# Optimization experiments

Measured on AMD Instinct MI355X. Metric: run time of the kernel, lower is better.

The kernel has to match this reference:

```python
import jax, jax.numpy as jnp
import numpy as np

BS, TLEN, NNODE, DIM = 32, 6, 4, 1500
HID = 128; D2 = 2 * HID
LSTMH, LSTMO, KCONV = 64, 128, 3
CONV_OUT = 191
DECAY = 0.7
WIN, STRIDES = (2, 2), (1, 2)
FEAT_IN = LSTMO * CONV_OUT  # 24448


def _bn(x, p, axis):
    # eval-mode BatchNorm: p = [gamma, beta, running_mean, running_var] stacked [4, C]
    sh = [1] * x.ndim; sh[axis] = -1
    g, b, m, v = (p[i].reshape(sh) for i in range(4))
    return (x - m) * (g * jax.lax.rsqrt(v + 1e-5)) + b


def _conv1d(x, w, pad):  # x [B,C,L], w [O,I,K]
    return jax.lax.conv_general_dilated(x, w, (1,), [(pad, pad)],
                                        dimension_numbers=('NCH', 'OIH', 'NCH'))


def _maxpool2(x):  # MaxPool1d(kernel=2, stride=2, padding=1) with -inf padding
    x = jnp.pad(x, ((0, 0), (0, 0), (1, 1)), constant_values=-jnp.inf)
    return jax.lax.reduce_window(x, -jnp.inf, jax.lax.max, (1, 1, 2), (1, 1, 2), 'VALID')


def _mpnn_block(x, w, s, gw, gb, bnA, tw, tb, bnM):
    # x: [bs, tlen, ns, d]; Conv_GraphST windowing + dot-graph + masked adj + 1-hop MPNN + mean pool
    bs, tlen, ns, d = x.shape
    nw = (tlen - w) // s + 1
    con = jnp.stack([x[:, j * s:j * s + w] for j in range(nw)], axis=1)  # [bs,nw,w,ns,d]
    Xc = con.reshape(bs * nw, w * ns, d)  # node index = t*ns + sensor (time-major)
    f = Xc @ gw + gb
    N = w * ns
    eye = jnp.eye(N, dtype=x.dtype)
    Adj = jnp.einsum('bnd,bmd->bnm', f, f)
    Adj = jax.nn.softmax(jax.nn.leaky_relu(Adj - eye * 1e8), axis=-1) + eye
    t = jnp.arange(N) // ns
    mask = DECAY ** jnp.abs(t[:, None] - t[None, :]).astype(x.dtype)  # Mask_Matrix decay
    Adj = Adj * mask
    Xb = _bn(Xc, bnA, -1)  # BN over feature channel (transpose-BN-transpose in torch)
    h = jnp.einsum('bnm,bmd->bnd', Adj, Xb) @ tw + tb
    h = jax.nn.leaky_relu(_bn(h, bnM, -1))
    return h.reshape(bs, nw, w, ns, -1).mean(axis=2)  # mean pool over window-time


def _pos_encoding(tlen, d):
    pos = jnp.arange(tlen, dtype=jnp.float32)[:, None]
    div = jnp.exp(jnp.arange(0, d, 2, dtype=jnp.float32) * (-np.log(100.0) / d))
    pe = jnp.zeros((tlen, d), jnp.float32)
    return pe.at[:, 0::2].set(jnp.sin(pos * div)).at[:, 1::2].set(jnp.cos(pos * div))


def reference(X, conv1_w, bn1, conv2_w, bn2, conv3_w, bn3,
              map2_w, map2_b, bn_map2,
              g1_w, g1_b, bnA1, th1_w, th1_b, bnM1,
              g2_w, g2_b, bnA2, th2_w, th2_b, bnM2,
              fc1_w, fc1_b, fc2_w, fc2_b, fc3_w, fc3_b, fc4_w, fc4_b):
    X = X.reshape(BS, TLEN, NNODE, -1)
    B = BS * TLEN * NNODE
    a = jnp.transpose(X.reshape(B, -1, 1), (0, 2, 1))  # [B,1,L]
    a = _maxpool2(jax.nn.relu(_bn(_conv1d(a, conv1_w, KCONV // 2), bn1, 1)))
    a = _maxpool2(jax.nn.relu(_bn(_conv1d(a, conv2_w, 2), bn2, 1)))
    a = _maxpool2(jax.nn.relu(_bn(_conv1d(a, conv3_w, 3), bn3, 1)))  # [B,LSTMO,CONV_OUT]
    a = a.reshape(B, -1)
    a = _bn(a @ map2_w + map2_b, bn_map2, -1)
    a = a.reshape(BS, TLEN, NNODE, D2)
    a = a + _pos_encoding(TLEN, D2)[None, :, None, :]  # PE over time, per (batch, node)
    out1 = _mpnn_block(a, WIN[0], STRIDES[0], g1_w, g1_b, bnA1, th1_w, th1_b, bnM1)  # [32,5,4,128]
    out2 = _mpnn_block(a, WIN[1], STRIDES[1], g2_w, g2_b, bnA2, th2_w, th2_b, bnM2)  # [32,3,4,128]
    feats = jnp.concatenate([out1.reshape(BS, -1), out2.reshape(BS, -1)], axis=-1)  # [32,4096]
    h = jax.nn.relu(feats @ fc1_w + fc1_b)
    h = jax.nn.relu(h @ fc2_w + fc2_b)
    h = jax.nn.relu(h @ fc3_w + fc3_b)
    return h @ fc4_w + fc4_b


def setup_inputs():
    key = jax.random.key(0)
    ks = iter(jax.random.split(key, 80))
    def rn(shape, scale=1.0):
        return scale * jax.random.normal(next(ks), shape, jnp.float32)
    def bn(c):
        return jnp.stack([1.0 + 0.1 * rn((c,)), 0.1 * rn((c,)), 0.1 * rn((c,)),
                          1.0 + 0.5 * jax.random.uniform(next(ks), (c,), jnp.float32)])
    def lin(i, o):
        return rn((i, o), 1.0 / np.sqrt(i))
    return {
        'X': rn((BS, TLEN, NNODE, DIM)),
        'conv1_w': rn((LSTMH, 1, KCONV), 0.3),
        'bn1': bn(LSTMH),
        'conv2_w': rn((2 * LSTMH, LSTMH, KCONV), 1.0 / np.sqrt(LSTMH * KCONV)),
        'bn2': bn(2 * LSTMH),
        'conv3_w': rn((LSTMO, 2 * LSTMH, KCONV), 1.0 / np.sqrt(2 * LSTMH * KCONV)),
        'bn3': bn(LSTMO),
        'map2_w': lin(FEAT_IN, D2), 'map2_b': rn((D2,), 0.01), 'bn_map2': bn(D2),
        'g1_w': lin(D2, D2), 'g1_b': rn((D2,), 0.01), 'bnA1': bn(D2),
        'th1_w': lin(D2, HID), 'th1_b': rn((HID,), 0.01), 'bnM1': bn(HID),
        'g2_w': lin(D2, D2), 'g2_b': rn((D2,), 0.01), 'bnA2': bn(D2),
        'th2_w': lin(D2, HID), 'th2_b': rn((HID,), 0.01), 'bnM2': bn(HID),
        'fc1_w': lin(4096, D2), 'fc1_b': rn((D2,), 0.01),
        'fc2_w': lin(D2, D2), 'fc2_b': rn((D2,), 0.01),
        'fc3_w': lin(D2, HID), 'fc3_b': rn((HID,), 0.01),
        'fc4_w': lin(HID, 5), 'fc4_b': rn((5,), 0.01),
    }
```

## Files before the change

### kernel.cpp

```cpp
#include <hip/hip_runtime.h>
#include <hip/hip_bf16.h>

#define L1X   1500
#define L1P   751
#define C1    64
#define L2P   377
#define C2    128
#define L3P   191
#define C3    128
#define FEATK 24448
#define D2    256
#define HIDN  128
#define KSTEPS 764
#define CHUNK 192

typedef __attribute__((ext_vector_type(8))) short bf16x8;
typedef __attribute__((ext_vector_type(4))) float f32x4;

__device__ __forceinline__ short f2bf(float x) {
    union { float f; unsigned u; } v; v.f = x;
    unsigned r = (v.u + 0x7FFFu + ((v.u >> 16) & 1u)) >> 16;
    return (short)r;
}
__device__ __forceinline__ float bf2f(short s) {
    union { float f; unsigned u; } v; v.u = ((unsigned)(unsigned short)s) << 16;
    return v.f;
}

template<int IC, int KB>
__global__ __launch_bounds__(256)
void k_wprep(const float* __restrict__ w, short* __restrict__ WtHi,
             short* __restrict__ WtLo)
{
    int idx = blockIdx.x * 256 + threadIdx.x;
    if (idx >= 3 * KB * 4 * 128 * 8) return;
    int i    = idx & 7;
    int rest = idx >> 3;
    int c    = rest & 127; rest >>= 7;
    int sub  = rest & 3;   rest >>= 2;
    int kb   = rest % KB;
    int tap  = rest / KB;
    int ic   = kb * 32 + sub * 8 + i;
    float x  = w[(c * IC + ic) * 3 + tap];
    short h  = f2bf(x);
    WtHi[idx] = h;
    WtLo[idx] = f2bf(x - bf2f(h));
}

__global__ __launch_bounds__(256)
void k_wmprep(const float* __restrict__ W, short* __restrict__ Wmhi,
              short* __restrict__ Wmlo)
{
    const int ks  = blockIdx.x >> 2;
    const int sub = blockIdx.x & 3;
    const int n   = threadIdx.x;
    const int kbase = ks * 32 + sub * 8;
    bf16x8 vh, vl;
    #pragma unroll
    for (int i = 0; i < 8; ++i) {
        int k = kbase + i;
        int c = k & 127, ip = k >> 7;
        float x = W[(size_t)(c * 191 + ip) * D2 + n];
        short h = f2bf(x);
        vh[i] = h;
        vl[i] = f2bf(x - bf2f(h));
    }
    size_t off = ((size_t)(ks * 4 + sub) * 256 + n) * 8;
    *(bf16x8*)(Wmhi + off) = vh;
    *(bf16x8*)(Wmlo + off) = vl;
}

__global__ __launch_bounds__(256)
void k_zero(float* __restrict__ p, int n)
{
    int i = blockIdx.x * 256 + threadIdx.x;
    if (i < n) p[i] = 0.f;
}

template<int IC, int KB, int CONVLEN, int POOLLEN, bool HL>
__device__ __forceinline__
void conv_mfma_core(const short* __restrict__ WtHi, const short* __restrict__ WtLo,
                    const short* lhi, const short* llo,
                    const float* sc, const float* bc,
                    float* __restrict__ outp, short* __restrict__ ohi,
                    short* __restrict__ olo, int P0)
{
    const int lane = threadIdx.x & 63;
    const int wave = threadIdx.x >> 6;
    const int l15  = lane & 15;
    const int sub  = lane >> 4;

    f32x4 acc[2][8];
    #pragma unroll
    for (int mf = 0; mf < 2; ++mf)
        #pragma unroll
        for (int nf = 0; nf < 8; ++nf)
            acc[mf][nf] = (f32x4){0.f, 0.f, 0.f, 0.f};

    #pragma unroll
    for (int tap = 0; tap < 3; ++tap) {
        #pragma unroll
        for (int kb = 0; kb < KB; ++kb) {
            bf16x8 ah[2], al[2];
            #pragma unroll
            for (int mf = 0; mf < 2; ++mf) {
                int r = wave * 32 + mf * 16 + l15 + tap;
                int chunk = (kb * 4 + sub) ^ (r & 7);
                int off = r * IC + chunk * 8;
                ah[mf] = *(const bf16x8*)(lhi + off);
                al[mf] = *(const bf16x8*)(llo + off);
            }
            const short* wbh = WtHi + (size_t)(((tap * KB + kb) * 4 + sub) * 128) * 8;
            const short* wbl = WtLo + (size_t)(((tap * KB + kb) * 4 + sub) * 128) * 8;
            #pragma unroll
            for (int nf = 0; nf < 8; ++nf) {
                bf16x8 bh = *(const bf16x8*)(wbh + (nf * 16 + l15) * 8);
                bf16x8 bl = *(const bf16x8*)(wbl + (nf * 16 + l15) * 8);
                #pragma unroll
                for (int mf = 0; mf < 2; ++mf) {
                    acc[mf][nf] = __builtin_amdgcn_mfma_f32_16x16x32_bf16(ah[mf], bh, acc[mf][nf], 0, 0, 0);
                    acc[mf][nf] = __builtin_amdgcn_mfma_f32_16x16x32_bf16(ah[mf], bl, acc[mf][nf], 0, 0, 0);
                    acc[mf][nf] = __builtin_amdgcn_mfma_f32_16x16x32_bf16(al[mf], bh, acc[mf][nf], 0, 0, 0);
                }
            }
        }
    }

    #pragma unroll
    for (int mf = 0; mf < 2; ++mf) {
        int mbase = wave * 32 + mf * 16 + sub * 4;
        #pragma unroll
        for (int nf = 0; nf < 8; ++nf) {
            int c = nf * 16 + l15;
            float s = sc[c], bb = bc[c];
            float v[4];
            #pragma unroll
            for (int rg = 0; rg < 4; ++rg) {
                int p = P0 + mbase + rg;
                float x = fmaxf(acc[mf][nf][rg] * s + bb, 0.f);
                v[rg] = (p >= 0 && p < CONVLEN) ? x : 0.f;
            }
            int i0 = (P0 + mbase + 1) >> 1;
            float u0 = fmaxf(v[0], v[1]);
            float u1 = fmaxf(v[2], v[3]);
            if constexpr (HL) {
                if (i0 < POOLLEN) {
                    short h = f2bf(u0);
                    ohi[(size_t)i0 * 128 + c] = h;
                    olo[(size_t)i0 * 128 + c] = f2bf(u0 - bf2f(h));
                }
                if (i0 + 1 < POOLLEN) {
                    short h = f2bf(u1);
                    ohi[(size_t)(i0 + 1) * 128 + c] = h;
                    olo[(size_t)(i0 + 1) * 128 + c] = f2bf(u1 - bf2f(h));
                }
            } else {
                if (i0 < POOLLEN)     outp[(size_t)i0 * 128 + c] = u0;
                if (i0 + 1 < POOLLEN) outp[(size_t)(i0 + 1) * 128 + c] = u1;
            }
        }
    }
}

__global__ __launch_bounds__(256)
void k_conv2_mfma(const float* __restrict__ X, const float* __restrict__ w1,
                  const float* __restrict__ bn1,
                  const short* __restrict__ Wt2hi, const short* __restrict__ Wt2lo,
                  const float* __restrict__ bn2, short* __restrict__ p2hi,
                  short* __restrict__ p2lo, int b_off)
{
    const int blk = blockIdx.x;
    const int bl  = blk / 6, t = blk % 6;
    const int b   = b_off + bl;
    const int P0  = 128 * t - 1;
    const int T0  = 128 * t - 3;
    const int X0  = 256 * t - 8;

    __shared__ __align__(16) float xw[264];
    __shared__ __align__(16) short t1h[130 * 64];
    __shared__ __align__(16) short t1l[130 * 64];
    __shared__ float sb1s[64], sb1b[64], sc2[128], bc2[128];

    const int tid = threadIdx.x;
    for (int g = tid; g < 262; g += 256) {
        int xi = X0 + g;
        xw[g] = (xi >= 0 && xi < L1X) ? X[(size_t)b * L1X + xi] : 0.f;
    }
    if (tid < 64) {
        float s = bn1[tid] * rsqrtf(bn1[192 + tid] + 1e-5f);
        sb1s[tid] = s;
        sb1b[tid] = bn1[64 + tid] - bn1[128 + tid] * s;
    }
    if (tid < 128) {
        float s = bn2[tid] * rsqrtf(bn2[384 + tid] + 1e-5f);
        sc2[tid] = s;
        bc2[tid] = bn2[128 + tid] - bn2[256 + tid] * s;
    }
    __syncthreads();

    for (int idx = tid; idx < 130 * 64; idx += 256) {
        int r = idx >> 6, c = idx & 63;
        int tt = T0 + r;
        float val = 0.f;
        if (tt >= 0 && tt <= 750) {
            float wk0 = w1[c * 3], wk1 = w1[c * 3 + 1], wk2 = w1[c * 3 + 2];
            float s = sb1s[c], bias = sb1b[c];
            float v0 = 0.f, v1 = 0.f;
            int li = 2 * r;
            if (tt >= 1)
                v0 = fmaxf((wk0 * xw[li] + wk1 * xw[li + 1] + wk2 * xw[li + 2]) * s + bias, 0.f);
            if (tt <= 749)
                v1 = fmaxf((wk0 * xw[li + 1] + wk1 * xw[li + 2] + wk2 * xw[li + 3]) * s + bias, 0.f);
            val = fmaxf(v0, v1);
        }
        short h = f2bf(val);
        int chunk = (c >> 3) ^ (r & 7);
        int off = r * 64 + chunk * 8 + (c & 7);
        t1h[off] = h;
        t1l[off] = f2bf(val - bf2f(h));
    }
    __syncthreads();

    conv_mfma_core<64, 2, 753, 377, true>(Wt2hi, Wt2lo, t1h, t1l, sc2, bc2,
                                          nullptr,
                                          p2hi + (size_t)bl * L2P * 128,
                                          p2lo + (size_t)bl * L2P * 128, P0);
}

__global__ __launch_bounds__(256)
void k_conv3_mfma(const short* __restrict__ p2hi, const short* __restrict__ p2lo,
                  const short* __restrict__ Wt3hi, const short* __restrict__ Wt3lo,
                  const float* __restrict__ bn3, short* __restrict__ p3hi,
                  short* __restrict__ p3lo, int b_off)
{
    const int blk = blockIdx.x;
    const int bl  = blk / 3, t = blk % 3;
    const int b   = b_off + bl;
    const int P0  = 128 * t - 1;
    const int I0  = 128 * t - 4;

    __shared__ __align__(16) short t2h[130 * 128];
    __shared__ __align__(16) short t2l[130 * 128];
    __shared__ float sc3[128], bc3[128];

    const int tid = threadIdx.x;
    if (tid < 128) {
        float s = bn3[tid] * rsqrtf(bn3[384 + tid] + 1e-5f);
        sc3[tid] = s;
        bc3[tid] = bn3[128 + tid] - bn3[256 + tid] * s;
    }

    const short* s2h = p2hi + (size_t)bl * L2P * 128;
    const short* s2l = p2lo + (size_t)bl * L2P * 128;
    for (int idx = tid; idx < 130 * 32; idx += 256) {
        int r = idx >> 5, q = idx & 31;
        int pr = I0 + r;
        short4 vh = make_short4(0, 0, 0, 0), vl = make_short4(0, 0, 0, 0);
        if (pr >= 0 && pr < L2P) {
            vh = *(const short4*)(s2h + (size_t)pr * 128 + q * 4);
            vl = *(const short4*)(s2l + (size_t)pr * 128 + q * 4);
        }
        int chunk = (q >> 1) ^ (r & 7);
        int off = r * 128 + chunk * 8 + (q & 1) * 4;
        *(short4*)(t2h + off) = vh;
        *(short4*)(t2l + off) = vl;
    }
    __syncthreads();

    conv_mfma_core<128, 4, 381, 191, true>(Wt3hi, Wt3lo, t2h, t2l, sc3, bc3,
                                           nullptr,
                                           p3hi + (size_t)b * FEATK,
                                           p3lo + (size_t)b * FEATK, P0);
}

__global__ __launch_bounds__(256)
void k_map2_mfma(const short* __restrict__ Ahi, const short* __restrict__ Alo,
                 const short* __restrict__ Wmhi, const short* __restrict__ Wmlo,
                 float* __restrict__ accum)
{
    const int kt   = blockIdx.x % 48;
    const int mt   = blockIdx.x / 48;
    const int tid  = threadIdx.x;
    const int lane = tid & 63, wave = tid >> 6;
    const int l15  = lane & 15, sub = lane >> 4;
    const int wm   = wave >> 1, wn = wave & 1;
    const int m0   = mt * 64;

    const int s0 = kt * 16;
    const int s1 = (s0 + 16 < KSTEPS) ? s0 + 16 : KSTEPS;

    __shared__ __align__(16) short Ah[2][64 * 40];
    __shared__ __align__(16) short Al[2][64 * 40];

    const int r  = tid >> 2;
    const int kb = tid & 3;
    const size_t abase = (size_t)(m0 + r) * FEATK + kb * 8;
    const int    lbase = r * 40 + kb * 8;

    f32x4 acc[2][8];
    #pragma unroll
    for (int mf = 0; mf < 2; ++mf)
        #pragma unroll
        for (int nf = 0; nf < 8; ++nf)
            acc[mf][nf] = (f32x4){0.f, 0.f, 0.f, 0.f};

    *(bf16x8*)&Ah[0][lbase] = *(const bf16x8*)(Ahi + abase + (size_t)s0 * 32);
    *(bf16x8*)&Al[0][lbase] = *(const bf16x8*)(Alo + abase + (size_t)s0 * 32);

    int cur = 0;
    for (int s = s0; s < s1; ++s) {
        __syncthreads();
        if (s + 1 < s1) {
            *(bf16x8*)&Ah[cur ^ 1][lbase] = *(const bf16x8*)(Ahi + abase + (size_t)(s + 1) * 32);
            *(bf16x8*)&Al[cur ^ 1][lbase] = *(const bf16x8*)(Alo + abase + (size_t)(s + 1) * 32);
        }
        bf16x8 ah[2], al[2];
        #pragma unroll
        for (int mf = 0; mf < 2; ++mf) {
            int off = (wm * 32 + mf * 16 + l15) * 40 + sub * 8;
            ah[mf] = *(const bf16x8*)&Ah[cur][off];
            al[mf] = *(const bf16x8*)&Al[cur][off];
        }
        const short* wb = Wmhi + ((size_t)(s * 4 + sub) * 256 + wn * 128) * 8;
        const short* wl = Wmlo + ((size_t)(s * 4 + sub) * 256 + wn * 128) * 8;
        #pragma unroll
        for (int nf = 0; nf < 8; ++nf) {
            bf16x8 bh = *(const bf16x8*)(wb + (nf * 16 + l15) * 8);
            bf16x8 bl = *(const bf16x8*)(wl + (nf * 16 + l15) * 8);
            #pragma unroll
            for (int mf = 0; mf < 2; ++mf) {
                acc[mf][nf] = __builtin_amdgcn_mfma_f32_16x16x32_bf16(ah[mf], bh, acc[mf][nf], 0, 0, 0);
                acc[mf][nf] = __builtin_amdgcn_mfma_f32_16x16x32_bf16(ah[mf], bl, acc[mf][nf], 0, 0, 0);
                acc[mf][nf] = __builtin_amdgcn_mfma_f32_16x16x32_bf16(al[mf], bh, acc[mf][nf], 0, 0, 0);
            }
        }
        cur ^= 1;
    }

    float* acct = accum + (size_t)(kt & 7) * 196608;
    #pragma unroll
    for (int mf = 0; mf < 2; ++mf) {
        int mrow = m0 + wm * 32 + mf * 16 + sub * 4;
        #pragma unroll
        for (int nf = 0; nf < 8; ++nf) {
            int n = wn * 128 + nf * 16 + l15;
            #pragma unroll
            for (int rg = 0; rg < 4; ++rg)
                atomicAdd(&acct[(size_t)(mrow + rg) * D2 + n], acc[mf][nf][rg]);
        }
    }
}

__global__ __launch_bounds__(256)
void k_map2fin(const float* __restrict__ accum, const float* __restrict__ mb,
               const float* __restrict__ bn, float* __restrict__ out)
{
    const int row = blockIdx.x;
    const int n   = threadIdx.x;
    float acc = 0.f;
    #pragma unroll
    for (int c = 0; c < 8; ++c)
        acc += accum[(size_t)c * 196608 + (size_t)row * D2 + n];

    float s    = bn[n] * rsqrtf(bn[768 + n] + 1e-5f);
    float beta = bn[256 + n];
    float mu   = bn[512 + n];
    float bias = mb[n];
    int   jj   = n >> 1;
    float freq = expf((float)(2 * jj) * (-4.605170185988092f / 256.f));
    int   t    = (row >> 2) % 6;
    float ang  = (float)t * freq;
    float pe   = (n & 1) ? cosf(ang) : sinf(ang);
    out[(size_t)row * D2 + n] = (acc + bias - mu) * s + beta + pe;
}

__global__ __launch_bounds__(256)
void k_mpnn(const float* __restrict__ a_pe, const float* __restrict__ gw,
            const float* __restrict__ gb, const float* __restrict__ bnA,
            const float* __restrict__ tw, const float* __restrict__ tb_,
            const float* __restrict__ bnM, float* __restrict__ feats,
            int nw, int stride, int base)
{
    const int g  = blockIdx.x;
    const int b  = g / nw, wi = g % nw;
    const int tid = threadIdx.x;

    __shared__ float Xc[8][256];
    __shared__ float Xb[8][256];
    __shared__ float Fs[8][256];
    __shared__ float Adj[8][8];
    __shared__ float hsm[8][128];

    for (int e = tid; e < 2048; e += 256) {
        int nn = e >> 8, d = e & 255;
        int tt = nn >> 2, sn = nn & 3;
        float v = a_pe[(((size_t)(b * 6) + (wi * stride + tt)) * 4 + sn) * D2 + d];
        Xc[nn][d] = v;
        float s = bnA[d] * rsqrtf(bnA[768 + d] + 1e-5f);
        Xb[nn][d] = (v - bnA[512 + d]) * s + bnA[256 + d];
    }
    __syncthreads();

    {
        const int d = tid;
        #pragma unroll
        for (int nn = 0; nn < 8; ++nn) {
            float acc = gb[d];
            for (int k = 0; k < 256; ++k) acc += Xc[nn][k] * gw[(size_t)k * D2 + d];
            Fs[nn][d] = acc;
        }
    }
    __syncthreads();

    if (tid < 64) {
        int nn = tid >> 3, m = tid & 7;
        float s = 0.f;
        for (int d = 0; d < 256; ++d) s += Fs[nn][d] * Fs[m][d];
        if (nn == m) s -= 1e8f;
        s = (s > 0.f) ? s : 0.01f * s;
        Adj[nn][m] = s;
    }
    __syncthreads();

    if (tid < 8) {
        int nn = tid;
        float mx = -1e30f;
        for (int m = 0; m < 8; ++m) mx = fmaxf(mx, Adj[nn][m]);
        float ex[8]; float sum = 0.f;
        for (int m = 0; m < 8; ++m) { ex[m] = expf(Adj[nn][m] - mx); sum += ex[m]; }
        float inv = 1.f / sum;
        for (int m = 0; m < 8; ++m) {
            float v = ex[m] * inv + ((nn == m) ? 1.f : 0.f);
            v *= ((nn >> 2) == (m >> 2)) ? 1.f : 0.7f;
            Adj[nn][m] = v;
        }
    }
    __syncthreads();

    {
        const int d = tid;
        float hm[8];
        #pragma unroll
        for (int nn = 0; nn < 8; ++nn) {
            float a = 0.f;
            #pragma unroll
            for (int m = 0; m < 8; ++m) a += Adj[nn][m] * Xb[m][d];
            hm[nn] = a;
        }
        #pragma unroll
        for (int nn = 0; nn < 8; ++nn) Fs[nn][d] = hm[nn];
    }
    __syncthreads();

    {
        const int o = tid & 127, half = tid >> 7;
        float ms  = bnM[o] * rsqrtf(bnM[384 + o] + 1e-5f);
        float mbe = bnM[128 + o], mmu = bnM[256 + o];
        #pragma unroll
        for (int q = 0; q < 4; ++q) {
            int nn = half + 2 * q;
            float acc = tb_[o];
            for (int d = 0; d < 256; ++d) acc += Fs[nn][d] * tw[(size_t)d * HIDN + o];
            float y = (acc - mmu) * ms + mbe;
            hsm[nn][o] = (y > 0.f) ? y : 0.01f * y;
        }
    }
    __syncthreads();

    for (int e = tid; e < 512; e += 256) {
        int sn = e >> 7, o = e & 127;
        feats[(size_t)b * 4096 + base + (wi * 4 + sn) * HIDN + o] =
            0.5f * (hsm[sn][o] + hsm[4 + sn][o]);
    }
}

__global__ __launch_bounds__(256)
void k_fc1(const float* __restrict__ feats, const float* __restrict__ w1f,
           float* __restrict__ partfc)
{
    const int kc = blockIdx.x >> 3;
    const int nc = blockIdx.x & 7;
    const int tid = threadIdx.x;

    __shared__ float fst[32 * 257];

    for (int idx = tid; idx < 32 * 256; idx += 256) {
        int r = idx >> 8, k = idx & 255;
        fst[r * 257 + k] = feats[(size_t)r * 4096 + kc * 256 + k];
    }
    __syncthreads();

    const int c  = tid & 31;
    const int rg = tid >> 5;
    const float* wp = w1f + (size_t)(kc * 256) * 256 + nc * 32 + c;

    float acc[4] = {0.f, 0.f, 0.f, 0.f};
    for (int k = 0; k < 256; ++k) {
        float wv = wp[(size_t)k * 256];
        #pragma unroll
        for (int j = 0; j < 4; ++j)
            acc[j] += fst[(rg * 4 + j) * 257 + k] * wv;
    }
    #pragma unroll
    for (int j = 0; j < 4; ++j)
        partfc[((size_t)kc * 32 + rg * 4 + j) * 256 + nc * 32 + c] = acc[j];
}

__global__ __launch_bounds__(256)
void k_fc_rest(const float* __restrict__ partfc,
               const float* __restrict__ b1f,
               const float* __restrict__ w2f, const float* __restrict__ b2f,
               const float* __restrict__ w3f, const float* __restrict__ b3f,
               const float* __restrict__ w4f, const float* __restrict__ b4f,
               float* __restrict__ out)
{
    const int b = blockIdx.x;
    const int n = threadIdx.x;
    __shared__ float h1[256], h2[256], h3[128];

    {
        float acc = b1f[n];
        #pragma unroll
        for (int kc = 0; kc < 16; ++kc)
            acc += partfc[((size_t)kc * 32 + b) * 256 + n];
        h1[n] = fmaxf(acc, 0.f);
    }
    __syncthreads();
    {
        float acc = b2f[n];
        for (int k = 0; k < 256; ++k) acc += h1[k] * w2f[(size_t)k * 256 + n];
        h2[n] = fmaxf(acc, 0.f);
    }
    __syncthreads();
    if (n < 128) {
        float acc = b3f[n];
        for (int k = 0; k < 256; ++k) acc += h2[k] * w3f[(size_t)k * 128 + n];
        h3[n] = fmaxf(acc, 0.f);
    }
    __syncthreads();
    if (n < 5) {
        float acc = b4f[n];
        for (int k = 0; k < 128; ++k) acc += h3[k] * w4f[(size_t)k * 5 + n];
        out[b * 5 + n] = acc;
    }
}

extern "C" void kernel_launch(void* const* d_in, const int* in_sizes, int n_in,
                              void* d_out, int out_size, void* d_ws, size_t ws_size,
                              hipStream_t stream)
{
    const float* X      = (const float*)d_in[0];
    const float* w1     = (const float*)d_in[1];
    const float* bn1    = (const float*)d_in[2];
    const float* w2     = (const float*)d_in[3];
    const float* bn2    = (const float*)d_in[4];
    const float* w3     = (const float*)d_in[5];
    const float* bn3    = (const float*)d_in[6];
    const float* map2w  = (const float*)d_in[7];
    const float* map2b  = (const float*)d_in[8];
    const float* bnm2   = (const float*)d_in[9];
    const float* g1w    = (const float*)d_in[10];
    const float* g1b    = (const float*)d_in[11];
    const float* bnA1   = (const float*)d_in[12];
    const float* th1w   = (const float*)d_in[13];
    const float* th1b   = (const float*)d_in[14];
    const float* bnM1   = (const float*)d_in[15];
    const float* g2w    = (const float*)d_in[16];
    const float* g2b    = (const float*)d_in[17];
    const float* bnA2   = (const float*)d_in[18];
    const float* th2w   = (const float*)d_in[19];
    const float* th2b   = (const float*)d_in[20];
    const float* bnM2   = (const float*)d_in[21];
    const float* fc1w   = (const float*)d_in[22];
    const float* fc1b   = (const float*)d_in[23];
    const float* fc2w   = (const float*)d_in[24];
    const float* fc2b   = (const float*)d_in[25];
    const float* fc3w   = (const float*)d_in[26];
    const float* fc3b   = (const float*)d_in[27];
    const float* fc4w   = (const float*)d_in[28];
    const float* fc4b   = (const float*)d_in[29];
    float* out = (float*)d_out;

    float* ws = (float*)d_ws;
    const size_t SZ_P2 = (size_t)CHUNK * L2P * 128;
    short* p2hi  = (short*)ws;
    short* p2lo  = p2hi + SZ_P2;
    short* Wmhi  = (short*)ws;
    short* Wmlo  = Wmhi + 6258688;
    float* accum = (float*)(Wmlo + 6258688);
    float* after  = ws + 9264384;
    short* p3hi   = (short*)after;
    short* p3lo   = p3hi + 18776064;
    float* a_pe   = (float*)(p3lo + 18776064);
    float* feats  = a_pe + 196608;
    short* Wt2hi  = (short*)(feats + 131072);
    short* Wt2lo  = Wt2hi + 24576;
    short* Wt3hi  = Wt2lo + 24576;
    short* Wt3lo  = Wt3hi + 49152;
    float* partfc = (float*)(Wt3lo + 49152);

    k_wprep<64, 2><<<96, 256, 0, stream>>>(w2, Wt2hi, Wt2lo);
    k_wprep<128, 4><<<192, 256, 0, stream>>>(w3, Wt3hi, Wt3lo);

    for (int boff = 0; boff < 768; boff += CHUNK) {
        k_conv2_mfma<<<CHUNK * 6, 256, 0, stream>>>(X, w1, bn1, Wt2hi, Wt2lo, bn2,
                                                    p2hi, p2lo, boff);
        k_conv3_mfma<<<CHUNK * 3, 256, 0, stream>>>(p2hi, p2lo, Wt3hi, Wt3lo, bn3,
                                                    p3hi, p3lo, boff);
    }
    k_wmprep<<<KSTEPS * 4, 256, 0, stream>>>(map2w, Wmhi, Wmlo);
    k_zero<<<(8 * 196608 + 255) / 256, 256, 0, stream>>>(accum, 8 * 196608);
    k_map2_mfma<<<576, 256, 0, stream>>>(p3hi, p3lo, Wmhi, Wmlo, accum);
    k_map2fin<<<768, 256, 0, stream>>>(accum, map2b, bnm2, a_pe);
    k_mpnn<<<160, 256, 0, stream>>>(a_pe, g1w, g1b, bnA1, th1w, th1b, bnM1,
                                    feats, 5, 1, 0);
    k_mpnn<<<96, 256, 0, stream>>>(a_pe, g2w, g2b, bnA2, th2w, th2b, bnM2,
                                   feats, 3, 2, 2560);
    k_fc1<<<128, 256, 0, stream>>>(feats, fc1w, partfc);
    k_fc_rest<<<32, 256, 0, stream>>>(partfc, fc1b, fc2w, fc2b, fc3w, fc3b,
                                      fc4w, fc4b, out);
}
```

Measured before the change: 679.0 us.

## Stage conv epilogue through LDS, vectorize conv1 and conv3 loads, merge MPNN launches

The conv MFMA epilogue now writes pooled bf16 hi/lo results into the shared input tile and then copies them to global memory as 16-byte vectors, replacing scattered 2-byte stores. The conv1 stage computes four channels per thread with float4 weight loads and short4 stores. The conv3 tile load is batched into registers with clamped addresses before being written to LDS. The two MPNN launches are merged into one grid. Together these aim to cut uncoalesced store traffic and launch overhead, at the cost of extra barriers and higher register pressure from the 17-entry staging arrays.

```diff
diff --git a/kernel.cpp b/kernel.cpp
--- a/kernel.cpp
+++ b/kernel.cpp
@@ -77,13 +77,12 @@
     if (i < n) p[i] = 0.f;
 }
 
-template<int IC, int KB, int CONVLEN, int POOLLEN, bool HL>
+template<int IC, int KB, int CONVLEN, int POOLLEN>
 __device__ __forceinline__
 void conv_mfma_core(const short* __restrict__ WtHi, const short* __restrict__ WtLo,
-                    const short* lhi, const short* llo,
+                    short* lhi, short* llo,
                     const float* sc, const float* bc,
-                    float* __restrict__ outp, short* __restrict__ ohi,
-                    short* __restrict__ olo, int P0)
+                    short* __restrict__ ohi, short* __restrict__ olo, int P0)
 {
     const int lane = threadIdx.x & 63;
     const int wave = threadIdx.x >> 6;
@@ -126,9 +125,11 @@
         }
     }
 
+    __syncthreads();
     #pragma unroll
     for (int mf = 0; mf < 2; ++mf) {
         int mbase = wave * 32 + mf * 16 + sub * 4;
+        int lr = mbase >> 1;
         #pragma unroll
         for (int nf = 0; nf < 8; ++nf) {
             int c = nf * 16 + l15;
@@ -140,24 +141,25 @@
                 float x = fmaxf(acc[mf][nf][rg] * s + bb, 0.f);
                 v[rg] = (p >= 0 && p < CONVLEN) ? x : 0.f;
             }
-            int i0 = (P0 + mbase + 1) >> 1;
             float u0 = fmaxf(v[0], v[1]);
             float u1 = fmaxf(v[2], v[3]);
-            if constexpr (HL) {
-                if (i0 < POOLLEN) {
-                    short h = f2bf(u0);
-                    ohi[(size_t)i0 * 128 + c] = h;
-                    olo[(size_t)i0 * 128 + c] = f2bf(u0 - bf2f(h));
-                }
-                if (i0 + 1 < POOLLEN) {
-                    short h = f2bf(u1);
-                    ohi[(size_t)(i0 + 1) * 128 + c] = h;
-                    olo[(size_t)(i0 + 1) * 128 + c] = f2bf(u1 - bf2f(h));
-                }
-            } else {
-                if (i0 < POOLLEN)     outp[(size_t)i0 * 128 + c] = u0;
-                if (i0 + 1 < POOLLEN) outp[(size_t)(i0 + 1) * 128 + c] = u1;
-            }
+            short h0 = f2bf(u0), h1 = f2bf(u1);
+            lhi[lr * 128 + c]       = h0;
+            llo[lr * 128 + c]       = f2bf(u0 - bf2f(h0));
+            lhi[(lr + 1) * 128 + c] = h1;
+            llo[(lr + 1) * 128 + c] = f2bf(u1 - bf2f(h1));
+        }
+    }
+    __syncthreads();
+
+    const int i0base = (P0 + 1) >> 1;
+    for (int e = threadIdx.x; e < 1024; e += 256) {
+        int row = e >> 4, g = e & 15;
+        if (i0base + row < POOLLEN) {
+            *(bf16x8*)(ohi + (size_t)(i0base + row) * 128 + g * 8) =
+                *(const bf16x8*)(lhi + row * 128 + g * 8);
+            *(bf16x8*)(olo + (size_t)(i0base + row) * 128 + g * 8) =
+                *(const bf16x8*)(llo + row * 128 + g * 8);
         }
     }
 }
@@ -198,33 +200,44 @@
     }
     __syncthreads();
 
-    for (int idx = tid; idx < 130 * 64; idx += 256) {
-        int r = idx >> 6, c = idx & 63;
+    for (int q2 = tid; q2 < 130 * 16; q2 += 256) {
+        int r  = q2 >> 4;
+        int cq = (q2 & 15) * 4;
         int tt = T0 + r;
-        float val = 0.f;
+        short4 sh = make_short4(0, 0, 0, 0), sl = make_short4(0, 0, 0, 0);
         if (tt >= 0 && tt <= 750) {
-            float wk0 = w1[c * 3], wk1 = w1[c * 3 + 1], wk2 = w1[c * 3 + 2];
-            float s = sb1s[c], bias = sb1b[c];
-            float v0 = 0.f, v1 = 0.f;
             int li = 2 * r;
-            if (tt >= 1)
-                v0 = fmaxf((wk0 * xw[li] + wk1 * xw[li + 1] + wk2 * xw[li + 2]) * s + bias, 0.f);
-            if (tt <= 749)
-                v1 = fmaxf((wk0 * xw[li + 1] + wk1 * xw[li + 2] + wk2 * xw[li + 3]) * s + bias, 0.f);
-            val = fmaxf(v0, v1);
-        }
-        short h = f2bf(val);
-        int chunk = (c >> 3) ^ (r & 7);
-        int off = r * 64 + chunk * 8 + (c & 7);
-        t1h[off] = h;
-        t1l[off] = f2bf(val - bf2f(h));
-    }
-    __syncthreads();
-
-    conv_mfma_core<64, 2, 753, 377, true>(Wt2hi, Wt2lo, t1h, t1l, sc2, bc2,
-                                          nullptr,
-                                          p2hi + (size_t)bl * L2P * 128,
-                                          p2lo + (size_t)bl * L2P * 128, P0);
+            float xa = xw[li], xb = xw[li + 1], xc = xw[li + 2], xd = xw[li + 3];
+            float4 wA = *(const float4*)(w1 + cq * 3);
+            float4 wB = *(const float4*)(w1 + cq * 3 + 4);
+            float4 wC = *(const float4*)(w1 + cq * 3 + 8);
+            float wv[4][3] = {{wA.x, wA.y, wA.z}, {wA.w, wB.x, wB.y},
+                              {wB.z, wB.w, wC.x}, {wC.y, wC.z, wC.w}};
+            #pragma unroll
+            for (int j = 0; j < 4; ++j) {
+                int c = cq + j;
+                float s = sb1s[c], bias = sb1b[c];
+                float v0 = 0.f, v1 = 0.f;
+                if (tt >= 1)
+                    v0 = fmaxf((wv[j][0] * xa + wv[j][1] * xb + wv[j][2] * xc) * s + bias, 0.f);
+                if (tt <= 749)
+                    v1 = fmaxf((wv[j][0] * xb + wv[j][1] * xc + wv[j][2] * xd) * s + bias, 0.f);
+                float val = fmaxf(v0, v1);
+                short h = f2bf(val);
+                ((short*)&sh)[j] = h;
+                ((short*)&sl)[j] = f2bf(val - bf2f(h));
+            }
+        }
+        int chunk = (cq >> 3) ^ (r & 7);
+        int off = r * 64 + chunk * 8 + (cq & 7);
+        *(short4*)(t1h + off) = sh;
+        *(short4*)(t1l + off) = sl;
+    }
+    __syncthreads();
+
+    conv_mfma_core<64, 2, 753, 377>(Wt2hi, Wt2lo, t1h, t1l, sc2, bc2,
+                                    p2hi + (size_t)bl * L2P * 128,
+                                    p2lo + (size_t)bl * L2P * 128, P0);
 }
 
 __global__ __launch_bounds__(256)
@@ -252,25 +265,36 @@
 
     const short* s2h = p2hi + (size_t)bl * L2P * 128;
     const short* s2l = p2lo + (size_t)bl * L2P * 128;
-    for (int idx = tid; idx < 130 * 32; idx += 256) {
+
+    unsigned long long rh[17], rl[17];
+    #pragma unroll
+    for (int k = 0; k < 17; ++k) {
+        int idx = tid + k * 256;
         int r = idx >> 5, q = idx & 31;
         int pr = I0 + r;
-        short4 vh = make_short4(0, 0, 0, 0), vl = make_short4(0, 0, 0, 0);
-        if (pr >= 0 && pr < L2P) {
-            vh = *(const short4*)(s2h + (size_t)pr * 128 + q * 4);
-            vl = *(const short4*)(s2l + (size_t)pr * 128 + q * 4);
-        }
-        int chunk = (q >> 1) ^ (r & 7);
-        int off = r * 128 + chunk * 8 + (q & 1) * 4;
-        *(short4*)(t2h + off) = vh;
-        *(short4*)(t2l + off) = vl;
-    }
-    __syncthreads();
-
-    conv_mfma_core<128, 4, 381, 191, true>(Wt3hi, Wt3lo, t2h, t2l, sc3, bc3,
-                                           nullptr,
-                                           p3hi + (size_t)b * FEATK,
-                                           p3lo + (size_t)b * FEATK, P0);
+        int prc = pr < 0 ? 0 : (pr >= L2P ? L2P - 1 : pr);
+        unsigned long long vh = *(const unsigned long long*)(s2h + (size_t)prc * 128 + q * 4);
+        unsigned long long vl = *(const unsigned long long*)(s2l + (size_t)prc * 128 + q * 4);
+        bool inb = (pr >= 0) && (pr < L2P) && (idx < 130 * 32);
+        rh[k] = inb ? vh : 0ull;
+        rl[k] = inb ? vl : 0ull;
+    }
+    #pragma unroll
+    for (int k = 0; k < 17; ++k) {
+        int idx = tid + k * 256;
+        if (idx < 130 * 32) {
+            int r = idx >> 5, q = idx & 31;
+            int chunk = (q >> 1) ^ (r & 7);
+            int off = r * 128 + chunk * 8 + (q & 1) * 4;
+            *(unsigned long long*)(t2h + off) = rh[k];
+            *(unsigned long long*)(t2l + off) = rl[k];
+        }
+    }
+    __syncthreads();
+
+    conv_mfma_core<128, 4, 381, 191>(Wt3hi, Wt3lo, t2h, t2l, sc3, bc3,
+                                     p3hi + (size_t)b * FEATK,
+                                     p3lo + (size_t)b * FEATK, P0);
 }
 
 __global__ __launch_bounds__(256)
@@ -375,13 +399,27 @@
 }
 
 __global__ __launch_bounds__(256)
-void k_mpnn(const float* __restrict__ a_pe, const float* __restrict__ gw,
-            const float* __restrict__ gb, const float* __restrict__ bnA,
-            const float* __restrict__ tw, const float* __restrict__ tb_,
-            const float* __restrict__ bnM, float* __restrict__ feats,
-            int nw, int stride, int base)
-{
-    const int g  = blockIdx.x;
+void k_mpnn_all(const float* __restrict__ a_pe,
+                const float* __restrict__ g1w, const float* __restrict__ g1b,
+                const float* __restrict__ bnA1, const float* __restrict__ th1w,
+                const float* __restrict__ th1b, const float* __restrict__ bnM1,
+                const float* __restrict__ g2w, const float* __restrict__ g2b,
+                const float* __restrict__ bnA2, const float* __restrict__ th2w,
+                const float* __restrict__ th2b, const float* __restrict__ bnM2,
+                float* __restrict__ feats)
+{
+    const bool second = blockIdx.x >= 160;
+    const int g    = second ? blockIdx.x - 160 : blockIdx.x;
+    const int nw   = second ? 3 : 5;
+    const int stride = second ? 2 : 1;
+    const int base = second ? 2560 : 0;
+    const float* gw  = second ? g2w : g1w;
+    const float* gb  = second ? g2b : g1b;
+    const float* bnA = second ? bnA2 : bnA1;
+    const float* tw  = second ? th2w : th1w;
+    const float* tb_ = second ? th2b : th1b;
+    const float* bnM = second ? bnM2 : bnM1;
+
     const int b  = g / nw, wi = g % nw;
     const int tid = threadIdx.x;
 
@@ -612,10 +650,8 @@
     k_zero<<<(8 * 196608 + 255) / 256, 256, 0, stream>>>(accum, 8 * 196608);
     k_map2_mfma<<<576, 256, 0, stream>>>(p3hi, p3lo, Wmhi, Wmlo, accum);
     k_map2fin<<<768, 256, 0, stream>>>(accum, map2b, bnm2, a_pe);
-    k_mpnn<<<160, 256, 0, stream>>>(a_pe, g1w, g1b, bnA1, th1w, th1b, bnM1,
-                                    feats, 5, 1, 0);
-    k_mpnn<<<96, 256, 0, stream>>>(a_pe, g2w, g2b, bnA2, th2w, th2b, bnM2,
-                                   feats, 3, 2, 2560);
+    k_mpnn_all<<<256, 256, 0, stream>>>(a_pe, g1w, g1b, bnA1, th1w, th1b, bnM1,
+                                        g2w, g2b, bnA2, th2w, th2b, bnM2, feats);
     k_fc1<<<128, 256, 0, stream>>>(feats, fc1w, partfc);
     k_fc_rest<<<32, 256, 0, stream>>>(partfc, fc1b, fc2w, fc2b, fc3w, fc3b,
                                       fc4w, fc4b, out);
```

Measured after the change: 730.2 us. +7.5%, slower.
